# Kernel optimization log

Hardware: AMD Instinct MI355X
Metric: run time of the kernel (lower is better)

## Reference

```python
import jax, jax.numpy as jnp
import numpy as np

B, K, I, H = 128, 512, 512, 512  # batch, seq_len, input_dim, hidden_dim


def setup_inputs() -> dict:
    key = jax.random.key(0)
    k1, k2, k3, k4, k5 = jax.random.split(key, 5)
    s_i = 1.0 / np.sqrt(H)
    return {
        "visual_seq": jax.random.normal(k1, (B, K, I), dtype=jnp.float32),
        # PyTorch GRU layout: gates stacked [r, z, n] along first dim
        "W_ih": jax.random.uniform(k2, (3 * H, I), minval=-s_i, maxval=s_i, dtype=jnp.float32),
        "W_hh": jax.random.uniform(k3, (3 * H, H), minval=-s_i, maxval=s_i, dtype=jnp.float32),
        "b_ih": jax.random.uniform(k4, (3 * H,), minval=-s_i, maxval=s_i, dtype=jnp.float32),
        "b_hh": jax.random.uniform(k5, (3 * H,), minval=-s_i, maxval=s_i, dtype=jnp.float32),
    }


def reference(visual_seq, W_ih, W_hh, b_ih, b_hh):
    # Fused single-layer GRU over all K steps (equivalent to the per-frame
    # torch loop with zero-initialized hidden state).
    Bs, Ks, _ = visual_seq.shape
    Hs = W_hh.shape[1]
    # Precompute input-gate projections for all timesteps: (K, B, 3H)
    x_gates = jnp.einsum('bki,gi->kbg', visual_seq, W_ih) + b_ih

    def step(h, xg):
        hg = h @ W_hh.T + b_hh                      # (B, 3H)
        xr, xz, xn = jnp.split(xg, 3, axis=-1)
        hr, hz, hn = jnp.split(hg, 3, axis=-1)
        r = jax.nn.sigmoid(xr + hr)
        z = jax.nn.sigmoid(xz + hz)
        n = jnp.tanh(xn + r * hn)
        h_new = (1.0 - z) * n + z * h
        return h_new, None

    h0 = jnp.zeros((Bs, Hs), dtype=visual_seq.dtype)
    h_final, _ = jax.lax.scan(step, h0, x_gates)
    return h_final  # (B, H) == h[-1] in the torch code
```

## Files before the change

kernel.cpp:

```cpp
#include <hip/hip_runtime.h>
#include <hip/hip_bf16.h>


#define CH 32
#define XG_BYTES (CH * 128 * 1536 * 4)
#define HB_BYTES (2 * 128 * 512 * 2)
#define HSTATE_BYTES (128 * 512 * 4)
#define CNT_STRIDE 16
#define CNT_BYTES (512 * 4 * CNT_STRIDE * 4)

typedef float  floatx4 __attribute__((ext_vector_type(4)));
typedef short  shortx8 __attribute__((ext_vector_type(8)));

__device__ __forceinline__ unsigned short f2bf(float f) {
    unsigned int u = __float_as_uint(f);
    u = (u + 0x7FFFu + ((u >> 16) & 1u)) >> 16;
    return (unsigned short)u;
}

__global__ __launch_bounds__(256, 1)
void gru_fused(const float* __restrict__ vis, const float* __restrict__ Wih,
               const float* __restrict__ bih, const float* __restrict__ Whh,
               const float* __restrict__ bhh,
               const float* __restrict__ xgR, float* __restrict__ xgW,
               unsigned short* __restrict__ hb, float* __restrict__ hstate,
               unsigned int* __restrict__ cnt, float* __restrict__ out,
               int kg0, int gemm_kg0, int do_rec, int do_gemm) {
    __shared__ unsigned short Ast[64][40];
    __shared__ unsigned short Bst[64][40];

    const int bx = blockIdx.x;
    const int t = threadIdx.x;
    const int wave = t >> 6, lane = t & 63, quad = lane >> 4, l16 = lane & 15;

    if (do_rec && bx < 64) {
        const int ug = bx & 15, bg = bx >> 4;
        const int u0 = ug * 32, b0 = bg * 32;
        const int mt = wave & 1, u16 = wave >> 1;
        const int b_base = b0 + mt * 16 + quad * 4;
        const int u = u0 + u16 * 16 + l16;

        shortx8 w[3][16];
        #pragma unroll
        for (int g = 0; g < 3; ++g) {
            #pragma unroll
            for (int kt = 0; kt < 16; ++kt) {
                const float* p = Whh + ((size_t)(g * 512 + u)) * 512 + kt * 32 + quad * 8;
                float4 a = *(const float4*)p;
                float4 b = *(const float4*)(p + 4);
                shortx8 v;
                v[0] = (short)f2bf(a.x); v[1] = (short)f2bf(a.y);
                v[2] = (short)f2bf(a.z); v[3] = (short)f2bf(a.w);
                v[4] = (short)f2bf(b.x); v[5] = (short)f2bf(b.y);
                v[6] = (short)f2bf(b.z); v[7] = (short)f2bf(b.w);
                w[g][kt] = v;
            }
        }
        const float bhr = bhh[u], bhz = bhh[512 + u], bhn = bhh[1024 + u];

        float hp[4];
        if (kg0 == 0) {
            hp[0] = hp[1] = hp[2] = hp[3] = 0.f;
        } else {
            #pragma unroll
            for (int reg = 0; reg < 4; ++reg) hp[reg] = hstate[(size_t)(b_base + reg) * 512 + u];
        }

        for (int s = 0; s < CH; ++s) {
            const int kg = kg0 + s;
            float xr[4], xz[4], xn[4];
            #pragma unroll
            for (int reg = 0; reg < 4; ++reg) {
                const float* xgp = xgR + ((size_t)s * 128 + b_base + reg) * 1536 + u;
                xr[reg] = xgp[0]; xz[reg] = xgp[512]; xn[reg] = xgp[1024];
            }

            union { unsigned long long u8[2]; shortx8 v; } af[16];
            if (kg > 0) {
                const unsigned int* fp = cnt + ((size_t)(kg - 1) * 4 + bg) * CNT_STRIDE;
                while (__hip_atomic_load(fp, __ATOMIC_RELAXED, __HIP_MEMORY_SCOPE_AGENT) < 16u)
                    __builtin_amdgcn_s_sleep(1);
                const unsigned short* hsrc = hb + (size_t)((kg - 1) & 1) * (128 * 512)
                                                + (size_t)(b0 + mt * 16 + l16) * 512 + quad * 8;
                #pragma unroll
                for (int kt = 0; kt < 16; ++kt) {
                    af[kt].u8[0] = __hip_atomic_load((const unsigned long long*)(hsrc + kt * 32),
                                                     __ATOMIC_RELAXED, __HIP_MEMORY_SCOPE_AGENT);
                    af[kt].u8[1] = __hip_atomic_load((const unsigned long long*)(hsrc + kt * 32 + 4),
                                                     __ATOMIC_RELAXED, __HIP_MEMORY_SCOPE_AGENT);
                }
            } else {
                #pragma unroll
                for (int kt = 0; kt < 16; ++kt) { af[kt].u8[0] = 0ull; af[kt].u8[1] = 0ull; }
            }

            floatx4 aR = {0,0,0,0}, aZ = {0,0,0,0}, aN = {0,0,0,0};
            #pragma unroll
            for (int kt = 0; kt < 16; ++kt) {
                aR = __builtin_amdgcn_mfma_f32_16x16x32_bf16(af[kt].v, w[0][kt], aR, 0, 0, 0);
                aZ = __builtin_amdgcn_mfma_f32_16x16x32_bf16(af[kt].v, w[1][kt], aZ, 0, 0, 0);
                aN = __builtin_amdgcn_mfma_f32_16x16x32_bf16(af[kt].v, w[2][kt], aN, 0, 0, 0);
            }

            unsigned short* hdst = hb + (size_t)(kg & 1) * (128 * 512);
            #pragma unroll
            for (int reg = 0; reg < 4; ++reg) {
                const float r = 1.f / (1.f + __expf(-(xr[reg] + aR[reg] + bhr)));
                const float z = 1.f / (1.f + __expf(-(xz[reg] + aZ[reg] + bhz)));
                const float n = tanhf(xn[reg] + r * (aN[reg] + bhn));
                const float h = (1.f - z) * n + z * hp[reg];
                hp[reg] = h;
                const float h_odd = __shfl_xor(h, 1);
                if (!(lane & 1)) {
                    unsigned int pk = (unsigned int)f2bf(h) | ((unsigned int)f2bf(h_odd) << 16);
                    __hip_atomic_store((unsigned int*)(hdst + (size_t)(b_base + reg) * 512 + u),
                                       pk, __ATOMIC_RELAXED, __HIP_MEMORY_SCOPE_AGENT);
                }
                if (kg == 511) out[(size_t)(b_base + reg) * 512 + u] = h;
            }
            __syncthreads();
            if (t == 0)
                __hip_atomic_fetch_add(cnt + ((size_t)kg * 4 + bg) * CNT_STRIDE, 1u,
                                       __ATOMIC_RELAXED, __HIP_MEMORY_SCOPE_AGENT);
        }

        #pragma unroll
        for (int reg = 0; reg < 4; ++reg)
            hstate[(size_t)(b_base + reg) * 512 + u] = hp[reg];
        return;
    }

    if (!do_gemm) return;
    const int NG = do_rec ? 192 : 256;
    const int gid = do_rec ? bx - 64 : bx;

    for (int T = gid; T < 1536; T += NG) {
        const int g0 = (T % 24) * 64;
        const int m0 = (T / 24) * 64;
        const int kc = m0 >> 7;
        const int b0 = m0 & 127;
        const int kg = gemm_kg0 + kc;

        floatx4 acc[4] = {{0,0,0,0},{0,0,0,0},{0,0,0,0},{0,0,0,0}};

        for (int ki = 0; ki < 16; ++ki) {
            const int i0 = ki * 32;
            #pragma unroll
            for (int rep = 0; rep < 2; ++rep) {
                const int r = (t >> 3) + rep * 32;
                const int c = (t & 7) * 4;
                float4 av = *(const float4*)(vis + ((size_t)(b0 + r) * 512 + kg) * 512 + i0 + c);
                ushort4 ab; ab.x = f2bf(av.x); ab.y = f2bf(av.y); ab.z = f2bf(av.z); ab.w = f2bf(av.w);
                *(ushort4*)&Ast[r][c] = ab;
                float4 bv = *(const float4*)(Wih + (size_t)(g0 + r) * 512 + i0 + c);
                ushort4 bb; bb.x = f2bf(bv.x); bb.y = f2bf(bv.y); bb.z = f2bf(bv.z); bb.w = f2bf(bv.w);
                *(ushort4*)&Bst[r][c] = bb;
            }
            __syncthreads();
            shortx8 afr = *(const shortx8*)(&Ast[wave * 16 + l16][quad * 8]);
            #pragma unroll
            for (int nb = 0; nb < 4; ++nb) {
                shortx8 bfr = *(const shortx8*)(&Bst[nb * 16 + l16][quad * 8]);
                acc[nb] = __builtin_amdgcn_mfma_f32_16x16x32_bf16(afr, bfr, acc[nb], 0, 0, 0);
            }
            __syncthreads();
        }
        #pragma unroll
        for (int nb = 0; nb < 4; ++nb) {
            const int g = g0 + nb * 16 + l16;
            const float bi = bih[g];
            #pragma unroll
            for (int reg = 0; reg < 4; ++reg) {
                const int m = m0 + wave * 16 + quad * 4 + reg;
                xgW[(size_t)m * 1536 + g] = acc[nb][reg] + bi;
            }
        }
    }
}

extern "C" void kernel_launch(void* const* d_in, const int* in_sizes, int n_in,
                              void* d_out, int out_size, void* d_ws, size_t ws_size,
                              hipStream_t stream) {
    const float* vis = (const float*)d_in[0];
    const float* Wih = (const float*)d_in[1];
    const float* Whh = (const float*)d_in[2];
    const float* bih = (const float*)d_in[3];
    const float* bhh = (const float*)d_in[4];
    float* out = (float*)d_out;

    char* ws = (char*)d_ws;
    float* xg0 = (float*)ws;
    float* xg1 = (float*)(ws + XG_BYTES);
    unsigned short* hb = (unsigned short*)(ws + 2 * XG_BYTES);
    float* hstate = (float*)(ws + 2 * XG_BYTES + HB_BYTES);
    unsigned int* cnt = (unsigned int*)(ws + 2 * XG_BYTES + HB_BYTES + HSTATE_BYTES);

    hipMemsetAsync(cnt, 0, CNT_BYTES, stream);

    float* bufs[2] = {xg0, xg1};

    gru_fused<<<256, 256, 0, stream>>>(vis, Wih, bih, Whh, bhh,
                                       xg0, xg0, hb, hstate, cnt, out,
                                       0, 0, 0, 1);
    for (int i = 0; i < 16; ++i) {
        gru_fused<<<256, 256, 0, stream>>>(vis, Wih, bih, Whh, bhh,
                                           bufs[i & 1], bufs[(i + 1) & 1],
                                           hb, hstate, cnt, out,
                                           i * CH, (i + 1) * CH, 1, (i < 15) ? 1 : 0);
    }
}
```

Measured before the change: 3.661 ms.

## Replace per-step block counters with per-wave monotonic tags and wave-level polling

```diff
diff --git a/kernel.cpp b/kernel.cpp
--- a/kernel.cpp
+++ b/kernel.cpp
@@ -6,8 +6,7 @@
 #define XG_BYTES (CH * 128 * 1536 * 4)
 #define HB_BYTES (2 * 128 * 512 * 2)
 #define HSTATE_BYTES (128 * 512 * 4)
-#define CNT_STRIDE 16
-#define CNT_BYTES (512 * 4 * CNT_STRIDE * 4)
+#define TAGS_BYTES (4 * 64 * 4)
 
 typedef float  floatx4 __attribute__((ext_vector_type(4)));
 typedef short  shortx8 __attribute__((ext_vector_type(8)));
@@ -24,7 +23,7 @@
                const float* __restrict__ bhh,
                const float* __restrict__ xgR, float* __restrict__ xgW,
                unsigned short* __restrict__ hb, float* __restrict__ hstate,
-               unsigned int* __restrict__ cnt, float* __restrict__ out,
+               unsigned int* __restrict__ tags, float* __restrict__ out,
                int kg0, int gemm_kg0, int do_rec, int do_gemm) {
     __shared__ unsigned short Ast[64][40];
     __shared__ unsigned short Bst[64][40];
@@ -39,6 +38,8 @@
         const int mt = wave & 1, u16 = wave >> 1;
         const int b_base = b0 + mt * 16 + quad * 4;
         const int u = u0 + u16 * 16 + l16;
+        unsigned int* mytag = tags + bg * 64 + ug * 4 + wave;
+        const unsigned int* tp = tags + bg * 64 + lane;
 
         shortx8 w[3][16];
         #pragma unroll
@@ -68,6 +69,13 @@
 
         for (int s = 0; s < CH; ++s) {
             const int kg = kg0 + s;
+
+            bool ready = true;
+            if (kg > 0) {
+                unsigned int tv = __hip_atomic_load(tp, __ATOMIC_RELAXED, __HIP_MEMORY_SCOPE_AGENT);
+                ready = __all((int)(tv >= (unsigned)kg));
+            }
+
             float xr[4], xz[4], xn[4];
             #pragma unroll
             for (int reg = 0; reg < 4; ++reg) {
@@ -77,9 +85,12 @@
 
             union { unsigned long long u8[2]; shortx8 v; } af[16];
             if (kg > 0) {
-                const unsigned int* fp = cnt + ((size_t)(kg - 1) * 4 + bg) * CNT_STRIDE;
-                while (__hip_atomic_load(fp, __ATOMIC_RELAXED, __HIP_MEMORY_SCOPE_AGENT) < 16u)
+                while (!ready) {
                     __builtin_amdgcn_s_sleep(1);
+                    unsigned int tv = __hip_atomic_load(tp, __ATOMIC_RELAXED, __HIP_MEMORY_SCOPE_AGENT);
+                    ready = __all((int)(tv >= (unsigned)kg));
+                }
+                __builtin_amdgcn_sched_barrier(0);
                 const unsigned short* hsrc = hb + (size_t)((kg - 1) & 1) * (128 * 512)
                                                 + (size_t)(b0 + mt * 16 + l16) * 512 + quad * 8;
                 #pragma unroll
@@ -118,10 +129,9 @@
                 }
                 if (kg == 511) out[(size_t)(b_base + reg) * 512 + u] = h;
             }
-            __syncthreads();
-            if (t == 0)
-                __hip_atomic_fetch_add(cnt + ((size_t)kg * 4 + bg) * CNT_STRIDE, 1u,
-                                       __ATOMIC_RELAXED, __HIP_MEMORY_SCOPE_AGENT);
+            if (lane == 0)
+                __hip_atomic_store(mytag, (unsigned int)(kg + 1),
+                                   __ATOMIC_RELEASE, __HIP_MEMORY_SCOPE_AGENT);
         }
 
         #pragma unroll
@@ -193,19 +203,19 @@
     float* xg1 = (float*)(ws + XG_BYTES);
     unsigned short* hb = (unsigned short*)(ws + 2 * XG_BYTES);
     float* hstate = (float*)(ws + 2 * XG_BYTES + HB_BYTES);
-    unsigned int* cnt = (unsigned int*)(ws + 2 * XG_BYTES + HB_BYTES + HSTATE_BYTES);
-
-    hipMemsetAsync(cnt, 0, CNT_BYTES, stream);
+    unsigned int* tags = (unsigned int*)(ws + 2 * XG_BYTES + HB_BYTES + HSTATE_BYTES);
+
+    hipMemsetAsync(tags, 0, TAGS_BYTES, stream);
 
     float* bufs[2] = {xg0, xg1};
 
     gru_fused<<<256, 256, 0, stream>>>(vis, Wih, bih, Whh, bhh,
-                                       xg0, xg0, hb, hstate, cnt, out,
+                                       xg0, xg0, hb, hstate, tags, out,
                                        0, 0, 0, 1);
     for (int i = 0; i < 16; ++i) {
         gru_fused<<<256, 256, 0, stream>>>(vis, Wih, bih, Whh, bhh,
                                            bufs[i & 1], bufs[(i + 1) & 1],
-                                           hb, hstate, cnt, out,
+                                           hb, hstate, tags, out,
                                            i * CH, (i + 1) * CH, 1, (i < 15) ? 1 : 0);
     }
 }
```

Result: slower. 6.547 ms (+78.8%).
